# Kernel tuning notes

Measured on AMD Instinct MI355X. Metric: run time of the kernel, lower is better.

## Reference

```python
import jax, jax.numpy as jnp
import numpy as np

K_NEIGHBORS = 32  # n_neighbors, eval mode -> displacement = 0


def setup_inputs() -> dict:
    key = jax.random.key(0)
    ks = jax.random.split(key, 9)
    B, N, F = 1024, 200000, 64
    C, H = 16, 128
    return {
        "x": jax.random.normal(ks[0], (B, F), jnp.float32),
        "X_data": jax.random.normal(ks[1], (N, F), jnp.float32),
        "y": jax.random.uniform(ks[2], (N,), jnp.float32),
        "W_gate": jax.random.normal(ks[3], (F + 1, C), jnp.float32) / np.sqrt(F + 1),
        "b_gate": jax.random.normal(ks[4], (C,), jnp.float32) * 0.01,
        "W1": jax.random.normal(ks[5], (C + F, H), jnp.float32) / np.sqrt(C + F),
        "b1": jax.random.normal(ks[6], (H,), jnp.float32) * 0.01,
        "W_last": jax.random.normal(ks[7], (H, 1), jnp.float32) / np.sqrt(H),
        "b_last": jax.random.normal(ks[8], (1,), jnp.float32) * 0.01,
    }


def reference(x, X_data, y, W_gate, b_gate, W1, b1, W_last, b_last):
    # Euclidean (p=2) cdist via the expanded form: ||a-b||^2 = ||a||^2 + ||b||^2 - 2 a.b
    d2 = (jnp.sum(x * x, axis=1, keepdims=True)
          + jnp.sum(X_data * X_data, axis=1)[None, :]
          - 2.0 * (x @ X_data.T))                      # [B, N]
    dist = jnp.sqrt(jnp.maximum(d2, 0.0))
    # torch.argsort(distances,1)[:, :k] == indices of k smallest distances
    _, idx = jax.lax.top_k(-dist, K_NEIGHBORS)          # [B, K]
    neighbors = X_data[idx]                             # [B, K, F] gather
    neighbors_y = y[idx][..., None]                     # [B, K, 1]
    nf = jnp.concatenate([neighbors, neighbors_y], axis=2)  # [B, K, F+1]
    gated = jnp.tanh(nf @ W_gate + b_gate)              # [B, K, C]
    agg = jnp.sum(gated, axis=1)                        # [B, C]
    o = jnp.concatenate([x, agg], axis=1)               # [B, F+C]
    o = jnp.tanh(o @ W1 + b1)                           # activation_function = tanh
    o = jax.nn.sigmoid(o @ W_last + b_last)             # [B, 1]
    return o
```

## Files before the change

### kernel.cpp

```cpp
#include <hip/hip_runtime.h>
#include <cstdint>

#define FDIM 64
#define KNN 32
#define NBUCKET 256
#define MAXCAP 2048
#define SEG 10
#define OCAP 512
#define BANDQ 96

typedef unsigned int u32;
typedef unsigned long long u64;
typedef __attribute__((ext_vector_type(8))) short bf16x8;
typedef __attribute__((ext_vector_type(4))) float f32x4;

__device__ __forceinline__ float load_query(const float* __restrict__ x, int q, float4* xv) {
    const float4* xp = (const float4*)(x + (size_t)q * FDIM);
    float n0 = 0.f, n1 = 0.f, n2 = 0.f, n3 = 0.f;
#pragma unroll
    for (int k = 0; k < 16; ++k) {
        float4 v = xp[k];
        xv[k] = v;
        n0 = fmaf(v.x, v.x, n0); n1 = fmaf(v.y, v.y, n1);
        n2 = fmaf(v.z, v.z, n2); n3 = fmaf(v.w, v.w, n3);
    }
    return (n0 + n1) + (n2 + n3);
}

__device__ __forceinline__ float dot_row(const float4* __restrict__ xv, const float* __restrict__ row) {
    const float4* rv = (const float4*)row;
    float d0 = 0.f, d1 = 0.f, d2 = 0.f, d3 = 0.f;
#pragma unroll
    for (int k = 0; k < 16; ++k) {
        float4 r = rv[k];
        float4 a = xv[k];
        d0 = fmaf(a.x, r.x, d0); d1 = fmaf(a.y, r.y, d1);
        d2 = fmaf(a.z, r.z, d2); d3 = fmaf(a.w, r.w, d3);
    }
    return (d0 + d1) + (d2 + d3);
}

__global__ __launch_bounds__(256) void k_xnorm(const float* __restrict__ X, float* __restrict__ Xn, int N) {
    int i = blockIdx.x * 256 + threadIdx.x;
    if (i >= N) return;
    const float4* r = (const float4*)(X + (size_t)i * FDIM);
    float d0 = 0.f, d1 = 0.f, d2 = 0.f, d3 = 0.f;
#pragma unroll
    for (int k = 0; k < 16; ++k) {
        float4 v = r[k];
        d0 = fmaf(v.x, v.x, d0); d1 = fmaf(v.y, v.y, d1);
        d2 = fmaf(v.z, v.z, d2); d3 = fmaf(v.w, v.w, d3);
    }
    Xn[i] = (d0 + d1) + (d2 + d3);
}

__global__ __launch_bounds__(256) void k_cvtT(const float* __restrict__ src, uint4* __restrict__ dst, int n_u4) {
    int i = blockIdx.x * 256 + threadIdx.x;
    if (i >= n_u4) return;
    int lane = i & 63;
    int kk = (i >> 6) & 1;
    int g = i >> 7;
    int row = g * 16 + (lane & 15);
    int col = kk * 32 + (lane >> 4) * 8;
    const float4* s = (const float4*)(src + (size_t)row * FDIM + col);
    float4 a = s[0], b = s[1];
    ushort o[8];
    const float* f = &a.x;
#pragma unroll
    for (int k = 0; k < 4; ++k) {
        u32 u = __float_as_uint(f[k]);
        o[k] = (ushort)((u + 0x7fffu + ((u >> 16) & 1u)) >> 16);
    }
    const float* gg = &b.x;
#pragma unroll
    for (int k = 0; k < 4; ++k) {
        u32 u = __float_as_uint(gg[k]);
        o[4 + k] = (ushort)((u + 0x7fffu + ((u >> 16) & 1u)) >> 16);
    }
    dst[i] = *(uint4*)o;
}

__global__ __launch_bounds__(256) void k_hist(const float* __restrict__ x, const float* __restrict__ X,
                                              const float* __restrict__ Xn, u32* __restrict__ hist,
                                              int N, int nsamp, int sj) {
    __shared__ unsigned char h8[NBUCKET * 256];
    int t = threadIdx.x;
    u32* h32 = (u32*)h8;
#pragma unroll
    for (int k = 0; k < 64; ++k) h32[k * 256 + t] = 0;
    __syncthreads();
    int q = blockIdx.x * 256 + t;
    float4 xv[16];
    float xn = load_query(x, q, xv);
    for (int j = 0; j < sj; ++j) {
        int s = blockIdx.y * sj + j;
        int p = s * 16;
        if (s < nsamp && p < N) {
            float dp = dot_row(xv, X + (size_t)p * FDIM);
            float d2 = fmaxf(xn + Xn[p] - 2.f * dp, 0.f);
            int b = min(NBUCKET - 1, (int)d2);
            int idx = b * 256 + t;
            unsigned char v = h8[idx];
            h8[idx] = (v == 255u) ? v : (unsigned char)(v + 1);
        }
    }
    __syncthreads();
#pragma unroll
    for (int w = 0; w < 128; ++w) {
        u32 v0 = h8[(2 * w) * 256 + t];
        u32 v1 = h8[(2 * w + 1) * 256 + t];
        if (v0 | v1) atomicAdd(&hist[(size_t)q * 128 + w], v0 | (v1 << 16));
    }
}

__global__ __launch_bounds__(256) void k_thresh(const u32* __restrict__ hist, float* __restrict__ Tq, int B) {
    int q = blockIdx.x * 256 + threadIdx.x;
    if (q >= B) return;
    const u32* h = hist + (size_t)q * 128;
    int cum = 0;
    float T = (float)NBUCKET;
    for (int w = 0; w < 128; ++w) {
        u32 v = h[w];
        cum += (int)(v & 0xffffu);
        if (cum >= KNN) { T = (float)(2 * w + 1); break; }
        cum += (int)(v >> 16);
        if (cum >= KNN) { T = (float)(2 * w + 2); break; }
    }
    Tq[q] = T + 2.0f;
}

__global__ __launch_bounds__(256, 3) void k_sample_d2(
        const uint4* __restrict__ xT, const uint4* __restrict__ XT,
        const float* __restrict__ qn, const float* __restrict__ Xn,
        unsigned char* __restrict__ d2s, int S) {
    int t = threadIdx.x;
    int w = t >> 6, lane = t & 63;
    int G = lane >> 4, r = lane & 15;
    int qg = blockIdx.x;
    int wq = qg * 128 + w * 32;
    int pb = blockIdx.y * 128;

    bf16x8 afr[2][2];
#pragma unroll
    for (int kk = 0; kk < 2; ++kk)
#pragma unroll
        for (int mi = 0; mi < 2; ++mi) {
            uint4 v = xT[(size_t)(((wq >> 4) + mi) * 2 + kk) * 64 + lane];
            afr[kk][mi] = *(bf16x8*)&v;
        }
    float qr[8];
#pragma unroll
    for (int e = 0; e < 8; ++e)
        qr[e] = qn[wq + (e >> 2) * 16 + G * 4 + (e & 3)];

#pragma unroll
    for (int half = 0; half < 2; ++half) {
        int nb = half * 4;
        bf16x8 bfr[4][2];
#pragma unroll
        for (int j = 0; j < 4; ++j) {
            int gp = (pb >> 4) + nb + j;
#pragma unroll
            for (int kk = 0; kk < 2; ++kk) {
                uint4 v = XT[(size_t)(gp * 2 + kk) * 64 + lane];
                bfr[j][kk] = *(bf16x8*)&v;
            }
        }
        float xnv[4];
#pragma unroll
        for (int j = 0; j < 4; ++j) xnv[j] = Xn[pb + (nb + j) * 16 + r];

        f32x4 acc[2][4];
#pragma unroll
        for (int mi = 0; mi < 2; ++mi)
#pragma unroll
            for (int j = 0; j < 4; ++j) acc[mi][j] = (f32x4){0.f, 0.f, 0.f, 0.f};
#pragma unroll
        for (int kk = 0; kk < 2; ++kk)
#pragma unroll
            for (int j = 0; j < 4; ++j) {
                acc[0][j] = __builtin_amdgcn_mfma_f32_16x16x32_bf16(afr[kk][0], bfr[j][kk], acc[0][j], 0, 0, 0);
                acc[1][j] = __builtin_amdgcn_mfma_f32_16x16x32_bf16(afr[kk][1], bfr[j][kk], acc[1][j], 0, 0, 0);
            }
#pragma unroll
        for (int j = 0; j < 4; ++j) {
            int p = pb + (nb + j) * 16 + r;
            float xnp = xnv[j];
#pragma unroll
            for (int e = 0; e < 8; ++e) {
                float d2a = qr[e] + fmaf(-2.f, acc[e >> 2][j][e & 3], xnp);
                int b = (int)d2a;
                b = b < 0 ? 0 : (b > 255 ? 255 : b);
                int q = wq + (e >> 2) * 16 + G * 4 + (e & 3);
                d2s[(size_t)q * S + p] = (unsigned char)b;
            }
        }
    }
}

__global__ __launch_bounds__(256) void k_thresh2(const unsigned char* __restrict__ d2s,
                                                 float* __restrict__ Tq, int S) {
    __shared__ u32 h[NBUCKET];
    int t = threadIdx.x;
    int q = blockIdx.x;
    h[t] = 0;
    __syncthreads();
    const u32* row = (const u32*)(d2s + (size_t)q * S);
    int n4 = S >> 2;
    for (int i = t; i < n4; i += 256) {
        u32 v = row[i];
        atomicAdd(&h[v & 255u], 1u);
        atomicAdd(&h[(v >> 8) & 255u], 1u);
        atomicAdd(&h[(v >> 16) & 255u], 1u);
        atomicAdd(&h[v >> 24], 1u);
    }
    __syncthreads();
    if (t == 0) {
        int cum = 0;
        float T = 256.0f;
        for (int b = 0; b < NBUCKET; ++b) {
            cum += (int)h[b];
            if (cum >= KNN) { T = (float)(b + 1); break; }
        }
        Tq[q] = T + 2.0f;
    }
}

__global__ __launch_bounds__(256, 3) void k_mfma_filter(
        const uint4* __restrict__ xT, const uint4* __restrict__ XT,
        const float* __restrict__ qn, const float* __restrict__ Xn,
        const float* __restrict__ Tf,
        u32* __restrict__ cnt_seg, u32* __restrict__ list_seg,
        u32* __restrict__ ocnt, u32* __restrict__ olist,
        int N, int nStripsPad, int strip) {
    __shared__ u32 ldsCnt[128];

    int t = threadIdx.x;
    int w = t >> 6, lane = t & 63;
    int G = lane >> 4, r = lane & 15;

    int bid = blockIdx.x;
    int qg = (bid >> 3) & 7;
    int sIdx = (bid & 7) | ((bid >> 6) << 3);
    int qbase = qg * 128;
    int wq = qbase + w * 32;

    if (t < 128) ldsCnt[t] = 0;
    __syncthreads();

    bf16x8 afr[2][2];
#pragma unroll
    for (int kk = 0; kk < 2; ++kk)
#pragma unroll
        for (int mi = 0; mi < 2; ++mi) {
            uint4 v = xT[(size_t)(((wq >> 4) + mi) * 2 + kk) * 64 + lane];
            afr[kk][mi] = *(bf16x8*)&v;
        }
    float Tr[8], qnr[8];
#pragma unroll
    for (int e = 0; e < 8; ++e) {
        int rl = wq + (e >> 2) * 16 + G * 4 + (e & 3);
        float qv = qn[rl];
        qnr[e] = qv;
        Tr[e] = Tf[rl] - qv;
    }

    u32* segBase = list_seg + ((size_t)qbase * nStripsPad + (size_t)sIdx) * SEG;

    for (int s = 0; s < strip; ++s) {
        int pb = (sIdx * strip + s) * 128;
        if (pb >= N) break;

#pragma unroll
        for (int half = 0; half < 2; ++half) {
            int nb = half * 4;
            bf16x8 bfr[4][2];
#pragma unroll
            for (int j = 0; j < 4; ++j) {
                int gp = (pb >> 4) + nb + j;
#pragma unroll
                for (int kk = 0; kk < 2; ++kk) {
                    uint4 v = XT[(size_t)(gp * 2 + kk) * 64 + lane];
                    bfr[j][kk] = *(bf16x8*)&v;
                }
            }
            float xnv[4];
#pragma unroll
            for (int j = 0; j < 4; ++j) xnv[j] = Xn[pb + (nb + j) * 16 + r];

            f32x4 acc[2][4];
#pragma unroll
            for (int mi = 0; mi < 2; ++mi)
#pragma unroll
                for (int j = 0; j < 4; ++j) acc[mi][j] = (f32x4){0.f, 0.f, 0.f, 0.f};
#pragma unroll
            for (int kk = 0; kk < 2; ++kk)
#pragma unroll
                for (int j = 0; j < 4; ++j) {
                    acc[0][j] = __builtin_amdgcn_mfma_f32_16x16x32_bf16(afr[kk][0], bfr[j][kk], acc[0][j], 0, 0, 0);
                    acc[1][j] = __builtin_amdgcn_mfma_f32_16x16x32_bf16(afr[kk][1], bfr[j][kk], acc[1][j], 0, 0, 0);
                }
#pragma unroll
            for (int j = 0; j < 4; ++j) {
                int p = pb + (nb + j) * 16 + r;
                float xnp = xnv[j];
                float dv[8];
                bool ce[8];
#pragma unroll
                for (int e = 0; e < 8; ++e) {
                    dv[e] = fmaf(-2.f, acc[e >> 2][j][e & 3], xnp);
                    ce[e] = dv[e] < Tr[e];
                }
                if ((ce[0] | ce[1] | ce[2] | ce[3] | ce[4] | ce[5] | ce[6] | ce[7]) && p < N) {
#pragma unroll
                    for (int e = 0; e < 8; ++e) {
                        if (ce[e]) {
                            float d2a = dv[e] + qnr[e];
                            d2a = d2a < 0.f ? 0.f : d2a;
                            u32 dq = (u32)(d2a * 32.f);
                            if (dq > 16383u) dq = 16383u;
                            u32 key = (dq << 18) | (u32)p;
                            int ql = w * 32 + (e >> 2) * 16 + G * 4 + (e & 3);
                            u32 slot = atomicAdd(&ldsCnt[ql], 1u);
                            if (slot < SEG) {
                                segBase[(size_t)ql * nStripsPad * SEG + slot] = key;
                            } else {
                                u32 gs = atomicAdd(&ocnt[qbase + ql], 1u);
                                if (gs < OCAP) olist[(size_t)(qbase + ql) * OCAP + gs] = key;
                            }
                        }
                    }
                }
            }
        }
    }

    __syncthreads();
    if (t < 128) cnt_seg[(size_t)(qbase + t) * nStripsPad + sIdx] = min(ldsCnt[t], (u32)SEG);
}

__global__ __launch_bounds__(256) void k_filter_scalar(const float* __restrict__ x, const float* __restrict__ X,
                                                       const float* __restrict__ Xn, const float* __restrict__ Tq,
                                                       u32* __restrict__ cnt, u32* __restrict__ list,
                                                       int N, int cap) {
    int t = threadIdx.x;
    int q = blockIdx.x * 256 + t;
    float4 xv[16];
    float xn = load_query(x, q, xv);
    float T = Tq[q];
    int base = blockIdx.y * 1024;
    int lim = min(1024, N - base);
    for (int j = 0; j < lim; ++j) {
        int p = base + j;
        float dp = dot_row(xv, X + (size_t)p * FDIM);
        float d2 = fmaxf(xn + Xn[p] - 2.f * dp, 0.f);
        if (d2 < T) {
            u32 slot = atomicAdd(&cnt[q], 1u);
            if (slot < (u32)cap) list[(size_t)q * cap + slot] = (u32)p;
        }
    }
}

__global__ __launch_bounds__(256) void k_final(const float* __restrict__ x, const float* __restrict__ X,
                                               const float* __restrict__ y, const float* __restrict__ Xn,
                                               const float* __restrict__ Wg, const float* __restrict__ bg,
                                               const float* __restrict__ W1, const float* __restrict__ b1,
                                               const float* __restrict__ Wl, const float* __restrict__ bl,
                                               const u32* __restrict__ cnt_seg, const u32* __restrict__ list_seg,
                                               const u32* __restrict__ ocnt, const u32* __restrict__ olist,
                                               const u32* __restrict__ cnt_flat, const u32* __restrict__ list_flat,
                                               float* __restrict__ out, int nStripsPad, int cap_flat, int flat,
                                               int N) {
    __shared__ u64 keys[MAXCAP];
    __shared__ u32 nsh;
    __shared__ u64 wk[4];
    __shared__ int wp[4];
    __shared__ u32 sel[KNN];
    __shared__ float gkc[KNN * 16];
    __shared__ float aggc[16];
    __shared__ float red[128];
    __shared__ u32 hist[2048];
    __shared__ u32 wtot[4];
    __shared__ u32 cutq_sh;
    __shared__ u32 nrs;

    int t = threadIdx.x;
    int w = t >> 6, lane = t & 63;
    int q = blockIdx.x;
    int m;

    if (flat) {
        m = (int)min(cnt_flat[q], (u32)cap_flat);
        const u32* lq = list_flat + (size_t)q * cap_flat;
        for (int i = t; i < m; i += 256) keys[i] = lq[i];
    } else {
        if (t == 0) nsh = 0;
        __syncthreads();
        for (int seg = t; seg < nStripsPad; seg += 256) {
            u32 c = cnt_seg[(size_t)q * nStripsPad + seg];
            if (c) {
                u32 base = atomicAdd(&nsh, c);
                const u32* sp = list_seg + ((size_t)q * nStripsPad + seg) * SEG;
                for (u32 j = 0; j < c; ++j) {
                    u32 idx = base + j;
                    if (idx < MAXCAP) keys[idx] = sp[j];
                }
            }
        }
        __syncthreads();
        int m0 = (int)min(nsh, (u32)MAXCAP);
        int oc = (int)min(ocnt[q], (u32)OCAP);
        for (int i = t; i < oc; i += 256)
            if (m0 + i < MAXCAP) keys[m0 + i] = olist[(size_t)q * OCAP + i];
        m = min(m0 + oc, MAXCAP);
    }
    __syncthreads();

    if (!flat) {
        for (int i = t; i < 2048; i += 256) hist[i] = 0;
        if (t == 0) cutq_sh = 0xFFFFFFFFu;
        __syncthreads();
        for (int i = t; i < m; i += 256) atomicAdd(&hist[((u32)keys[i]) >> 21], 1u);
        __syncthreads();
        u32 s = 0;
#pragma unroll
        for (int j = 0; j < 8; ++j) s += hist[t * 8 + j];
        u32 run = s;
#pragma unroll
        for (int off = 1; off < 64; off <<= 1) {
            u32 v = __shfl_up(run, off);
            if (lane >= off) run += v;
        }
        if (lane == 63) wtot[w] = run;
        __syncthreads();
        u32 wo = 0;
#pragma unroll
        for (int v = 0; v < 4; ++v) wo += (v < w) ? wtot[v] : 0u;
        u32 inc = wo + run;
        u32 exc = inc - s;
        if (exc < (u32)KNN && inc >= (u32)KNN) {
            u32 cum = exc;
#pragma unroll
            for (int j = 0; j < 8; ++j) {
                cum += hist[t * 8 + j];
                if (cum >= (u32)KNN) { cutq_sh = (u32)(((t * 8 + j + 1) << 3) + BANDQ); break; }
            }
        }
    }
    if (t == 0) nrs = 0;
    __syncthreads();
    u32 cutq = flat ? 0xFFFFFFFFu : cutq_sh;

    u32* cand = hist;
    for (int i = t; i < m; i += 256) {
        u32 k = (u32)keys[i];
        if ((k >> 18) <= cutq) cand[atomicAdd(&nrs, 1u)] = k & 0x3FFFFu;
    }
    __syncthreads();
    int mr = (int)min(nrs, (u32)MAXCAP);

    {
        int ch = lane & 15;
        int rsub = lane >> 4;
        float4 xq4 = ((const float4*)(x + (size_t)q * FDIM))[ch];
        float xs = fmaf(xq4.x, xq4.x, fmaf(xq4.y, xq4.y, fmaf(xq4.z, xq4.z, xq4.w * xq4.w)));
        xs += __shfl_xor(xs, 1);
        xs += __shfl_xor(xs, 2);
        xs += __shfl_xor(xs, 4);
        xs += __shfl_xor(xs, 8);
        float xn = xs;
        for (int base = w * 32; base < mr; base += 128) {
            int ri[8]; u32 pp[8]; bool val[8]; float4 vv[8];
#pragma unroll
            for (int u = 0; u < 8; ++u) {
                ri[u] = base + u * 4 + rsub;
                val[u] = ri[u] < mr;
                pp[u] = val[u] ? cand[ri[u]] : 0u;
            }
#pragma unroll
            for (int u = 0; u < 8; ++u)
                vv[u] = ((const float4*)(X + (size_t)pp[u] * FDIM))[ch];
#pragma unroll
            for (int u = 0; u < 8; ++u) {
                float part = fmaf(xq4.x, vv[u].x, fmaf(xq4.y, vv[u].y, fmaf(xq4.z, vv[u].z, xq4.w * vv[u].w)));
                part += __shfl_xor(part, 1);
                part += __shfl_xor(part, 2);
                part += __shfl_xor(part, 4);
                part += __shfl_xor(part, 8);
                if (val[u] && ch == 0) {
                    float d2 = fmaxf(xn + Xn[pp[u]] - 2.f * part, 0.f);
                    keys[ri[u]] = ((u64)__float_as_uint(d2) << 32) | pp[u];
                }
            }
        }
    }
    __syncthreads();

    if (mr <= 512) {
        if (w == 0) {
            u64 rk[8];
#pragma unroll
            for (int i = 0; i < 8; ++i) {
                int idx = lane + (i << 6);
                rk[i] = (idx < mr) ? keys[idx] : ~0ull;
            }
            for (int r = 0; r < KNN; ++r) {
                u64 bk = ~0ull;
                int bs = 0;
#pragma unroll
                for (int i = 0; i < 8; ++i)
                    if (rk[i] < bk) { bk = rk[i]; bs = i; }
                int bo = lane;
#pragma unroll
                for (int off = 1; off < 64; off <<= 1) {
                    u64 ok = __shfl_xor(bk, off);
                    int oo = __shfl_xor(bo, off);
                    if (ok < bk) { bk = ok; bo = oo; }
                }
                if (lane == bo) rk[bs] = ~0ull;
                if (lane == 0) sel[r] = (u32)bk;
            }
        }
        __syncthreads();
    } else {
        for (int r = 0; r < KNN; ++r) {
            u64 bk = ~0ull;
            int bp = -1;
            for (int i = t; i < mr; i += 256) {
                u64 k = keys[i];
                if (k < bk) { bk = k; bp = i; }
            }
#pragma unroll
            for (int off = 32; off > 0; off >>= 1) {
                u64 ok = __shfl_down(bk, off);
                int op = __shfl_down(bp, off);
                if (ok < bk) { bk = ok; bp = op; }
            }
            if (lane == 0) { wk[w] = bk; wp[w] = bp; }
            __syncthreads();
            if (t == 0) {
                u64 fb = wk[0];
                int fp = wp[0];
                for (int v = 1; v < 4; ++v)
                    if (wk[v] < fb) { fb = wk[v]; fp = wp[v]; }
                sel[r] = (u32)(fb & 0xffffffffu);
                if (fp >= 0) keys[fp] = ~0ull;
            }
            __syncthreads();
        }
    }

    int c = t & 15, kk = t >> 4;
#pragma unroll
    for (int rep = 0; rep < 2; ++rep) {
        int k = kk + 16 * rep;
        int nb = min((int)sel[k], N - 1);
        const float* Xr = X + (size_t)nb * FDIM;
        float acc = bg[c];
#pragma unroll
        for (int f = 0; f < FDIM; ++f) acc = fmaf(Xr[f], Wg[f * 16 + c], acc);
        acc = fmaf(y[nb], Wg[FDIM * 16 + c], acc);
        gkc[k * 16 + c] = tanhf(acc);
    }
    __syncthreads();
    if (t < 16) {
        float s = 0.f;
#pragma unroll
        for (int k = 0; k < KNN; ++k) s += gkc[k * 16 + t];
        aggc[t] = s;
    }
    __syncthreads();
    if (t < 128) {
        const float* xq = x + (size_t)q * FDIM;
        float acc = b1[t];
#pragma unroll
        for (int f = 0; f < FDIM; ++f) acc = fmaf(xq[f], W1[f * 128 + t], acc);
#pragma unroll
        for (int cc2 = 0; cc2 < 16; ++cc2) acc = fmaf(aggc[cc2], W1[(FDIM + cc2) * 128 + t], acc);
        red[t] = tanhf(acc) * Wl[t];
    }
    __syncthreads();
    for (int off = 64; off > 0; off >>= 1) {
        if (t < off) red[t] += red[t + off];
        __syncthreads();
    }
    if (t == 0) out[q] = 1.f / (1.f + expf(-(red[0] + bl[0])));
}

extern "C" void kernel_launch(void* const* d_in, const int* in_sizes, int n_in,
                              void* d_out, int out_size, void* d_ws, size_t ws_size,
                              hipStream_t stream) {
    const float* x  = (const float*)d_in[0];
    const float* X  = (const float*)d_in[1];
    const float* y  = (const float*)d_in[2];
    const float* Wg = (const float*)d_in[3];
    const float* bg = (const float*)d_in[4];
    const float* W1 = (const float*)d_in[5];
    const float* b1 = (const float*)d_in[6];
    const float* Wl = (const float*)d_in[7];
    const float* bl = (const float*)d_in[8];
    float* out = (float*)d_out;

    int B = in_sizes[0] / FDIM;
    int N = in_sizes[1] / FDIM;

    const int strip = 8;
    int nTiles = (N + 127) / 128;
    int nStrips = (nTiles + strip - 1) / strip;
    nStrips = (nStrips + 7) & ~7;
    int nStripsPad = nStrips;
    int Npad = nStrips * strip * 128;

    char* w = (char*)d_ws;
    size_t off = 0;
    auto alloc = [&](size_t bytes) { void* p = w + off; off += (bytes + 255) & ~(size_t)255; return p; };
    float* Xn  = (float*)alloc((size_t)Npad * 4);
    float* qn  = (float*)alloc((size_t)B * 4);
    u32* hist  = (u32*)alloc((size_t)B * 512);
    float* Tq  = (float*)alloc((size_t)B * 4);
    u32* cnt   = (u32*)alloc((size_t)B * 4);

    size_t xTB = (size_t)B * 128;
    size_t XTB = (size_t)(Npad / 16) * 2048;
    size_t segCntB = (size_t)B * nStripsPad * 4;
    size_t segListB = (size_t)B * nStripsPad * SEG * 4;
    size_t ocntB = (size_t)B * 4;
    size_t olistB = (size_t)B * OCAP * 4;
    size_t rem = (ws_size > off) ? ws_size - off : 0;
    bool mfma_path = rem >= xTB + XTB + segCntB + segListB + ocntB + olistB + 4096;

    uint4* xT = nullptr; uint4* XT = nullptr;
    u32 *cnt_seg = nullptr, *list_seg = nullptr, *ocnt = nullptr, *olist = nullptr;
    u32* list_flat = nullptr; unsigned char* d2s = nullptr;
    int cap_flat = 64, Stiles = 0;
    if (mfma_path) {
        xT = (uint4*)alloc(xTB);
        XT = (uint4*)alloc(XTB);
        cnt_seg  = (u32*)alloc(segCntB);
        list_seg = (u32*)alloc(segListB);
        ocnt     = (u32*)alloc(ocntB);
        olist    = (u32*)alloc(olistB);
        rem = (ws_size > off) ? ws_size - off : 0;
        size_t st = rem / ((size_t)B * 128);
        Stiles = st > 198 ? 198 : (int)st;
        int maxFull = N / 128;
        if (Stiles > maxFull) Stiles = maxFull;
        if (Stiles >= 96) d2s = (unsigned char*)alloc((size_t)Stiles * 128 * B);
        else Stiles = 0;
    } else {
        size_t c = rem / ((size_t)B * 4);
        cap_flat = c > MAXCAP ? MAXCAP : (int)c;
        if (cap_flat < 64) cap_flat = 64;
        list_flat = (u32*)alloc((size_t)B * cap_flat * 4);
    }

    k_xnorm<<<dim3((N + 255) / 256), 256, 0, stream>>>(X, Xn, N);
    k_xnorm<<<dim3((B + 255) / 256), 256, 0, stream>>>(x, qn, B);

    if (mfma_path) {
        hipMemsetAsync(ocnt, 0, ocntB, stream);
        hipMemsetAsync(Xn + N, 0, (size_t)(Npad - N) * 4, stream);
        size_t realXT = (size_t)(N / 16) * 2048;
        hipMemsetAsync((char*)XT + realXT, 0, XTB - realXT, stream);

        int nxu4 = B * 8, nXu4 = N * 8;
        k_cvtT<<<dim3((nxu4 + 255) / 256), 256, 0, stream>>>(x, xT, nxu4);
        k_cvtT<<<dim3((nXu4 + 255) / 256), 256, 0, stream>>>(X, XT, nXu4);

        if (Stiles > 0) {
            int S = Stiles * 128;
            k_sample_d2<<<dim3(8, Stiles), 256, 0, stream>>>(xT, XT, qn, Xn, d2s, S);
            k_thresh2<<<dim3(B), 256, 0, stream>>>(d2s, Tq, S);
        } else {
            hipMemsetAsync(hist, 0, (size_t)B * 512, stream);
            int nsamp = (N + 15) / 16;
            int chunks = 128;
            int sj = (nsamp + chunks - 1) / chunks;
            k_hist<<<dim3(B / 256, chunks), 256, 0, stream>>>(x, X, Xn, hist, N, nsamp, sj);
            k_thresh<<<dim3((B + 255) / 256), 256, 0, stream>>>(hist, Tq, B);
        }

        k_mfma_filter<<<dim3(8 * nStrips), 256, 0, stream>>>(
            xT, XT, qn, Xn, Tq, cnt_seg, list_seg, ocnt, olist, N, nStripsPad, strip);

        k_final<<<dim3(B), 256, 0, stream>>>(x, X, y, Xn, Wg, bg, W1, b1, Wl, bl,
                                             cnt_seg, list_seg, ocnt, olist,
                                             nullptr, nullptr, out, nStripsPad, 0, 0, N);
    } else {
        hipMemsetAsync(cnt, 0, (size_t)B * 4, stream);
        hipMemsetAsync(hist, 0, (size_t)B * 512, stream);
        int nsamp = (N + 15) / 16;
        int chunks = 128;
        int sj = (nsamp + chunks - 1) / chunks;
        k_hist<<<dim3(B / 256, chunks), 256, 0, stream>>>(x, X, Xn, hist, N, nsamp, sj);
        k_thresh<<<dim3((B + 255) / 256), 256, 0, stream>>>(hist, Tq, B);
        k_filter_scalar<<<dim3(B / 256, (N + 1023) / 1024), 256, 0, stream>>>(
            x, X, Xn, Tq, cnt, list_flat, N, cap_flat);
        k_final<<<dim3(B), 256, 0, stream>>>(x, X, y, Xn, Wg, bg, W1, b1, Wl, bl,
                                             nullptr, nullptr, nullptr, nullptr,
                                             cnt, list_flat, out, nStripsPad, cap_flat, 1, N);
    }
}
```

Measured before the change: 261.8 us.

## Double-buffer data tiles into LDS via direct global-to-LDS loads in MFMA filter

The MFMA filter kernel now streams each 128-point strip of the transposed bf16 dataset into a two-slot LDS buffer using global_load_lds, prefetching the next strip while the current one is processed. Before, B fragments were loaded straight from global memory into registers. The distance offset is also folded into the MFMA accumulator init (-0.5*||X||^2), so the threshold test is a single compare against a prescaled threshold. The occupancy hint rises from 3 to 4 blocks per SM. The cost is 32KB of LDS per block plus a barrier on every strip, which may limit occupancy. Waits on the async LDS loads rely on the barrier.

Result: no change. 261.8 us (-0.0%).

```diff
diff --git a/kernel.cpp b/kernel.cpp
--- a/kernel.cpp
+++ b/kernel.cpp
@@ -13,6 +13,13 @@
 typedef unsigned long long u64;
 typedef __attribute__((ext_vector_type(8))) short bf16x8;
 typedef __attribute__((ext_vector_type(4))) float f32x4;
+
+__device__ __forceinline__ void gload_lds16(const void* g, void* l) {
+    __builtin_amdgcn_global_load_lds(
+        (const __attribute__((address_space(1))) unsigned int*)g,
+        (__attribute__((address_space(3))) unsigned int*)l,
+        16, 0, 0);
+}
 
 __device__ __forceinline__ float load_query(const float* __restrict__ x, int q, float4* xv) {
     const float4* xp = (const float4*)(x + (size_t)q * FDIM);
@@ -226,13 +233,14 @@
     }
 }
 
-__global__ __launch_bounds__(256, 3) void k_mfma_filter(
+__global__ __launch_bounds__(256, 4) void k_mfma_filter(
         const uint4* __restrict__ xT, const uint4* __restrict__ XT,
         const float* __restrict__ qn, const float* __restrict__ Xn,
         const float* __restrict__ Tf,
         u32* __restrict__ cnt_seg, u32* __restrict__ list_seg,
         u32* __restrict__ ocnt, u32* __restrict__ olist,
         int N, int nStripsPad, int strip) {
+    __shared__ uint4 sbuf[2][1024];
     __shared__ u32 ldsCnt[128];
 
     int t = threadIdx.x;
@@ -256,82 +264,104 @@
             uint4 v = xT[(size_t)(((wq >> 4) + mi) * 2 + kk) * 64 + lane];
             afr[kk][mi] = *(bf16x8*)&v;
         }
-    float Tr[8], qnr[8];
+    float nT[8], qnr[8];
 #pragma unroll
     for (int e = 0; e < 8; ++e) {
         int rl = wq + (e >> 2) * 16 + G * 4 + (e & 3);
         float qv = qn[rl];
         qnr[e] = qv;
-        Tr[e] = Tf[rl] - qv;
+        nT[e] = -0.5f * (Tf[rl] - qv);
     }
 
     u32* segBase = list_seg + ((size_t)qbase * nStripsPad + (size_t)sIdx) * SEG;
 
-    for (int s = 0; s < strip; ++s) {
-        int pb = (sIdx * strip + s) * 128;
-        if (pb >= N) break;
-
-#pragma unroll
-        for (int half = 0; half < 2; ++half) {
-            int nb = half * 4;
-            bf16x8 bfr[4][2];
-#pragma unroll
-            for (int j = 0; j < 4; ++j) {
-                int gp = (pb >> 4) + nb + j;
-#pragma unroll
-                for (int kk = 0; kk < 2; ++kk) {
-                    uint4 v = XT[(size_t)(gp * 2 + kk) * 64 + lane];
-                    bfr[j][kk] = *(bf16x8*)&v;
+    int pb0 = sIdx * strip * 128;
+    int ntl = (pb0 < N) ? strip : 0;
+
+    if (ntl > 0) {
+        {
+            const char* src = (const char*)XT + (size_t)(pb0 >> 4) * 2048 + w * 1024 + lane * 16;
+            char* dst = (char*)&sbuf[0][0] + w * 1024;
+            gload_lds16(src, dst);
+            gload_lds16(src + 4096, dst + 4096);
+            gload_lds16(src + 8192, dst + 8192);
+            gload_lds16(src + 12288, dst + 12288);
+        }
+        __syncthreads();
+
+        for (int s = 0; s < ntl; ++s) {
+            int pb = pb0 + s * 128;
+            if (s + 1 < ntl) {
+                const char* src = (const char*)XT + (size_t)((pb + 128) >> 4) * 2048 + w * 1024 + lane * 16;
+                char* dst = (char*)&sbuf[(s + 1) & 1][0] + w * 1024;
+                gload_lds16(src, dst);
+                gload_lds16(src + 4096, dst + 4096);
+                gload_lds16(src + 8192, dst + 8192);
+                gload_lds16(src + 12288, dst + 12288);
+            }
+            const uint4* cur = &sbuf[s & 1][0];
+
+#pragma unroll
+            for (int half = 0; half < 2; ++half) {
+                int nb = half * 4;
+                bf16x8 bfr[4][2];
+#pragma unroll
+                for (int j = 0; j < 4; ++j) {
+#pragma unroll
+                    for (int kk = 0; kk < 2; ++kk) {
+                        uint4 v = cur[((nb + j) * 2 + kk) * 64 + lane];
+                        bfr[j][kk] = *(bf16x8*)&v;
+                    }
                 }
-            }
-            float xnv[4];
-#pragma unroll
-            for (int j = 0; j < 4; ++j) xnv[j] = Xn[pb + (nb + j) * 16 + r];
-
-            f32x4 acc[2][4];
-#pragma unroll
-            for (int mi = 0; mi < 2; ++mi)
-#pragma unroll
-                for (int j = 0; j < 4; ++j) acc[mi][j] = (f32x4){0.f, 0.f, 0.f, 0.f};
-#pragma unroll
-            for (int kk = 0; kk < 2; ++kk)
+                float xnv[4], ai[4];
 #pragma unroll
                 for (int j = 0; j < 4; ++j) {
-                    acc[0][j] = __builtin_amdgcn_mfma_f32_16x16x32_bf16(afr[kk][0], bfr[j][kk], acc[0][j], 0, 0, 0);
-                    acc[1][j] = __builtin_amdgcn_mfma_f32_16x16x32_bf16(afr[kk][1], bfr[j][kk], acc[1][j], 0, 0, 0);
+                    xnv[j] = Xn[pb + (nb + j) * 16 + r];
+                    ai[j] = -0.5f * xnv[j];
                 }
-#pragma unroll
-            for (int j = 0; j < 4; ++j) {
-                int p = pb + (nb + j) * 16 + r;
-                float xnp = xnv[j];
-                float dv[8];
-                bool ce[8];
-#pragma unroll
-                for (int e = 0; e < 8; ++e) {
-                    dv[e] = fmaf(-2.f, acc[e >> 2][j][e & 3], xnp);
-                    ce[e] = dv[e] < Tr[e];
-                }
-                if ((ce[0] | ce[1] | ce[2] | ce[3] | ce[4] | ce[5] | ce[6] | ce[7]) && p < N) {
-#pragma unroll
-                    for (int e = 0; e < 8; ++e) {
-                        if (ce[e]) {
-                            float d2a = dv[e] + qnr[e];
-                            d2a = d2a < 0.f ? 0.f : d2a;
-                            u32 dq = (u32)(d2a * 32.f);
-                            if (dq > 16383u) dq = 16383u;
-                            u32 key = (dq << 18) | (u32)p;
-                            int ql = w * 32 + (e >> 2) * 16 + G * 4 + (e & 3);
-                            u32 slot = atomicAdd(&ldsCnt[ql], 1u);
-                            if (slot < SEG) {
-                                segBase[(size_t)ql * nStripsPad * SEG + slot] = key;
-                            } else {
-                                u32 gs = atomicAdd(&ocnt[qbase + ql], 1u);
-                                if (gs < OCAP) olist[(size_t)(qbase + ql) * OCAP + gs] = key;
+
+                f32x4 acc[2][4];
+#pragma unroll
+                for (int mi = 0; mi < 2; ++mi)
+#pragma unroll
+                    for (int j = 0; j < 4; ++j) acc[mi][j] = (f32x4){ai[j], ai[j], ai[j], ai[j]};
+#pragma unroll
+                for (int kk = 0; kk < 2; ++kk)
+#pragma unroll
+                    for (int j = 0; j < 4; ++j) {
+                        acc[0][j] = __builtin_amdgcn_mfma_f32_16x16x32_bf16(afr[kk][0], bfr[j][kk], acc[0][j], 0, 0, 0);
+                        acc[1][j] = __builtin_amdgcn_mfma_f32_16x16x32_bf16(afr[kk][1], bfr[j][kk], acc[1][j], 0, 0, 0);
+                    }
+#pragma unroll
+                for (int j = 0; j < 4; ++j) {
+                    int p = pb + (nb + j) * 16 + r;
+                    bool ce[8];
+#pragma unroll
+                    for (int e = 0; e < 8; ++e)
+                        ce[e] = acc[e >> 2][j][e & 3] > nT[e];
+                    if ((ce[0] | ce[1] | ce[2] | ce[3] | ce[4] | ce[5] | ce[6] | ce[7]) && p < N) {
+#pragma unroll
+                        for (int e = 0; e < 8; ++e) {
+                            if (ce[e]) {
+                                float d2a = fmaf(-2.f, acc[e >> 2][j][e & 3], qnr[e]);
+                                d2a = d2a < 0.f ? 0.f : d2a;
+                                u32 dq = (u32)(d2a * 32.f);
+                                if (dq > 16383u) dq = 16383u;
+                                u32 key = (dq << 18) | (u32)p;
+                                int ql = w * 32 + (e >> 2) * 16 + G * 4 + (e & 3);
+                                u32 slot = atomicAdd(&ldsCnt[ql], 1u);
+                                if (slot < SEG) {
+                                    segBase[(size_t)ql * nStripsPad * SEG + slot] = key;
+                                } else {
+                                    u32 gs = atomicAdd(&ocnt[qbase + ql], 1u);
+                                    if (gs < OCAP) olist[(size_t)(qbase + ql) * OCAP + gs] = key;
+                                }
                             }
                         }
                     }
                 }
             }
+            __syncthreads();
         }
     }
 
```
